# Kernel tuning notes

Measured on AMD Instinct MI355X. Metric: run time of the kernel, lower is better.

## Reference

```python
import jax, jax.numpy as jnp
import numpy as np

N = 100000   # nodes
E = 1600000  # edges
C = 128      # num_features == out_channels
L = 3        # num_layers


def setup_inputs() -> dict:
    key = jax.random.key(0)
    ks = jax.random.split(key, 7)
    x = jax.random.normal(ks[0], (N, C), dtype=jnp.float32)
    edge_index = jax.random.randint(ks[1], (2, E), 0, N, dtype=jnp.int64)
    # GatedGraphConv per-layer linear weights [L, C, C]
    weight = jax.random.normal(ks[2], (L, C, C), dtype=jnp.float32) / np.sqrt(C)
    # shared GRUCell params (torch layout: [3C, C] rows = r, z, n)
    w_ih = jax.random.normal(ks[3], (3 * C, C), dtype=jnp.float32) / np.sqrt(C)
    w_hh = jax.random.normal(ks[4], (3 * C, C), dtype=jnp.float32) / np.sqrt(C)
    b_ih = jax.random.normal(ks[5], (3 * C,), dtype=jnp.float32) * 0.01
    b_hh = jax.random.normal(ks[6], (3 * C,), dtype=jnp.float32) * 0.01
    return {"x": x, "edge_index": edge_index, "weight": weight,
            "w_ih": w_ih, "w_hh": w_hh, "b_ih": b_ih, "b_hh": b_hh}


def _gru_cell(inp, h, w_ih, w_hh, b_ih, b_hh):
    gi = inp @ w_ih.T + b_ih  # [N, 3C]
    gh = h @ w_hh.T + b_hh    # [N, 3C]
    i_r, i_z, i_n = jnp.split(gi, 3, axis=1)
    h_r, h_z, h_n = jnp.split(gh, 3, axis=1)
    r = jax.nn.sigmoid(i_r + h_r)
    z = jax.nn.sigmoid(i_z + h_z)
    n = jnp.tanh(i_n + r * h_n)
    return (1.0 - z) * n + z * h


def reference(x, edge_index, weight, w_ih, w_hh, b_ih, b_hh):
    src, dst = edge_index[0], edge_index[1]
    n_nodes = x.shape[0]
    # mean aggregation denominators (in-degree, 0-degree nodes -> 0 output)
    counts = jax.ops.segment_sum(jnp.ones(src.shape[0], dtype=x.dtype), dst,
                                 num_segments=n_nodes)
    denom = jnp.maximum(counts, 1.0)[:, None]
    h = x
    for i in range(weight.shape[0]):
        m = h @ weight[i]                                   # [N, C]
        agg = jax.ops.segment_sum(m[src], dst, num_segments=n_nodes) / denom
        h = _gru_cell(agg, h, w_ih, w_hh, b_ih, b_hh)
    # x.mean(1).unsqueeze(1) -> [N, 1], then tanh
    return jnp.tanh(jnp.mean(h, axis=1, keepdims=True))
```

## Files before the change

### kernel.cpp

```cpp
#include <hip/hip_runtime.h>
#include <math.h>

#define NN 100000
#define NE 1600000
#define CC 128
#define C3 384
#define SCAN_B 256
#define SCAN_NB ((NN + SCAN_B - 1) / SCAN_B)

typedef __attribute__((ext_vector_type(4))) float f4;
typedef __attribute__((ext_vector_type(8))) short s8;

__device__ __forceinline__ float sigmoidf_(float x) { return 1.0f / (1.0f + __expf(-x)); }
__device__ __forceinline__ float tanhf_(float x) { return 2.0f / (1.0f + __expf(-2.0f * x)) - 1.0f; }

__device__ __forceinline__ short f2bf(float x) {
    unsigned u = __float_as_uint(x);
    unsigned r = (u + 0x7fffu + ((u >> 16) & 1u)) >> 16;
    return (short)r;
}
__device__ __forceinline__ float bf2f(short s) {
    return __uint_as_float(((unsigned)(unsigned short)s) << 16);
}

__device__ __forceinline__ int detect_flag(const int* e32) {
    int allz = 1;
#pragma unroll
    for (int i = 0; i < 32; i++)
        if (e32[2 * i + 1] != 0) allz = 0;
    return allz;
}

__device__ __forceinline__ int edge_val(const void* edges, int f, long long idx) {
    return f ? (int)((const long long*)edges)[idx] : ((const int*)edges)[idx];
}

__global__ void k_count(const void* __restrict__ edges, int* __restrict__ counts) {
    __shared__ int sf;
    if (threadIdx.x == 0) sf = detect_flag((const int*)edges);
    __syncthreads();
    int f = sf;
    int e = blockIdx.x * blockDim.x + threadIdx.x;
    if (e < NE) {
        int d = edge_val(edges, f, (long long)NE + e);
        atomicAdd(&counts[d], 1);
    }
}

__global__ void k_scan1(const int* __restrict__ counts, int* __restrict__ bsum) {
    __shared__ int red[4];
    int t = threadIdx.x;
    int i = blockIdx.x * SCAN_B + t;
    int v = (i < NN) ? counts[i] : 0;
#pragma unroll
    for (int off = 32; off; off >>= 1) v += __shfl_down(v, off);
    if ((t & 63) == 0) red[t >> 6] = v;
    __syncthreads();
    if (t == 0) bsum[blockIdx.x] = red[0] + red[1] + red[2] + red[3];
}

__global__ void k_scan2(const int* __restrict__ bsum, int* __restrict__ boff,
                        int* __restrict__ coarse_cursor) {
    __shared__ int lds[512];
    int t = threadIdx.x;
    int v = (t < SCAN_NB) ? bsum[t] : 0;
    lds[t] = v;
    __syncthreads();
    for (int off = 1; off < 512; off <<= 1) {
        int u = (t >= off) ? lds[t - off] : 0;
        __syncthreads();
        lds[t] += u;
        __syncthreads();
    }
    if (t < SCAN_NB) {
        int ex = lds[t] - v;
        boff[t] = ex;
        coarse_cursor[t] = ex;
    }
}

__global__ void k_scan3(const int* __restrict__ counts, const int* __restrict__ boff,
                        int* __restrict__ rowptr, float* __restrict__ inv_denom) {
    __shared__ int lds[SCAN_B];
    int t = threadIdx.x;
    int i = blockIdx.x * SCAN_B + t;
    int v = (i < NN) ? counts[i] : 0;
    lds[t] = v;
    __syncthreads();
    for (int off = 1; off < SCAN_B; off <<= 1) {
        int u = (t >= off) ? lds[t - off] : 0;
        __syncthreads();
        lds[t] += u;
        __syncthreads();
    }
    if (i < NN) {
        rowptr[i] = boff[blockIdx.x] + lds[t] - v;
        inv_denom[i] = 1.0f / (float)((v > 1) ? v : 1);
    }
    if (i == 0) rowptr[NN] = NE;
}

__global__ __launch_bounds__(1024) void k_part(const void* __restrict__ edges,
                                               int* __restrict__ coarse_cursor,
                                               uint2* __restrict__ tmp) {
    __shared__ int hist[SCAN_NB];
    __shared__ int base[SCAN_NB];
    __shared__ int sf;
    int t = threadIdx.x;
    if (t == 0) sf = detect_flag((const int*)edges);
    long long e0 = (long long)blockIdx.x * 8192;

    for (int c = t; c < SCAN_NB; c += 1024) hist[c] = 0;
    __syncthreads();
    int f = sf;

    int src[8], dst[8];
#pragma unroll
    for (int i = 0; i < 8; i++) {
        long long e = e0 + i * 1024 + t;
        if (e < NE) {
            src[i] = edge_val(edges, f, e);
            dst[i] = edge_val(edges, f, NE + e);
            atomicAdd(&hist[dst[i] >> 8], 1);
        } else {
            dst[i] = -1;
        }
    }
    __syncthreads();
    for (int c = t; c < SCAN_NB; c += 1024) {
        int h = hist[c];
        base[c] = (h > 0) ? atomicAdd(&coarse_cursor[c], h) : 0;
        hist[c] = 0;
    }
    __syncthreads();
#pragma unroll
    for (int i = 0; i < 8; i++) {
        if (dst[i] >= 0) {
            int c = dst[i] >> 8;
            int off = atomicAdd(&hist[c], 1);
            tmp[base[c] + off] = make_uint2((unsigned)src[i], (unsigned)dst[i]);
        }
    }
}

__global__ void k_fine(const uint2* __restrict__ tmp, const int* __restrict__ rowptr,
                       int* __restrict__ csr_src) {
    __shared__ int cur[256];
    int c = blockIdx.x;
    int t = threadIdx.x;
    int d = c * 256 + t;
    cur[t] = (d <= NN) ? rowptr[d < NN ? d : NN] : NE;
    __syncthreads();
    int start = rowptr[c * 256];
    int endd = (c * 256 + 256 <= NN) ? rowptr[c * 256 + 256] : NE;
    for (int p = start + t; p < endd; p += 256) {
        uint2 pr = tmp[p];
        int slot = atomicAdd(&cur[pr.y & 255], 1);
        csr_src[slot] = (int)pr.x;
    }
}

__global__ void k_prep(const float* __restrict__ weight, const float* __restrict__ w_ih,
                       const float* __restrict__ w_hh, const float* __restrict__ b_ih,
                       const float* __restrict__ b_hh,
                       short* __restrict__ B1hi, short* __restrict__ B2hi,
                       float* __restrict__ bvec) {
    const int P1 = 3 * C3 * CC;
    int gid = blockIdx.x * blockDim.x + threadIdx.x;
    if (gid < P1) {
        int i = gid / (C3 * CC);
        int rem = gid % (C3 * CC);
        int j = rem / CC;
        int k = rem % CC;
        const float* Wr = weight + i * CC * CC + k * CC;
        const float* ir = w_ih + j * CC;
        float v = 0.f;
#pragma unroll 4
        for (int c = 0; c < CC; c++) v += Wr[c] * ir[c];
        short hi = f2bf(v);
        if (j < 256) B1hi[i * 65536 + j * 256 + k] = hi;
        else B2hi[i * 32768 + (j - 256) * 128 + k] = hi;
    } else if (gid < 2 * P1) {
        int g = gid - P1;
        int i = g / (C3 * CC);
        int rem = g % (C3 * CC);
        int j = rem / CC;
        int k = rem % CC;
        short hi = f2bf(w_hh[j * CC + k]);
        if (j < 256) B1hi[i * 65536 + j * 256 + 128 + k] = hi;
        else B2hi[i * 32768 + (j - 256 + 128) * 128 + k] = hi;
    } else if (gid < 2 * P1 + 512) {
        int j = gid - 2 * P1;
        float v;
        if (j < 256) v = b_ih[j] + b_hh[j];
        else if (j < 384) v = b_ih[j];
        else v = b_hh[j - 128];
        bvec[j] = v;
    }
}

__global__ void k_cvt(const float* __restrict__ x, unsigned short* __restrict__ hhi,
                      unsigned short* __restrict__ hlo) {
    long long g = ((long long)blockIdx.x * 256 + threadIdx.x) * 8;
    float4 v0 = *(const float4*)(x + g);
    float4 v1 = *(const float4*)(x + g + 4);
    float f[8] = {v0.x, v0.y, v0.z, v0.w, v1.x, v1.y, v1.z, v1.w};
    s8 oh, ol;
#pragma unroll
    for (int q = 0; q < 8; q++) {
        short hi = f2bf(f[q]);
        oh[q] = hi;
        ol[q] = f2bf(f[q] - bf2f(hi));
    }
    *(s8*)(hhi + g) = oh;
    *(s8*)(hlo + g) = ol;
}

__global__ __launch_bounds__(512, 8) void k_fused(
    const unsigned short* __restrict__ hhi_i, const unsigned short* __restrict__ hlo_i,
    unsigned short* __restrict__ hhi_o, unsigned short* __restrict__ hlo_o,
    const int* __restrict__ rowptr, const int* __restrict__ csr_src,
    const float* __restrict__ inv_denom,
    const short* __restrict__ B1hi, const short* __restrict__ B2hi,
    const float* __restrict__ bvec, float* __restrict__ out) {
    __shared__ short Ahi[8192];
    __shared__ short Alo[8192];
    __shared__ float osum[32];
    int t = threadIdx.x;
    long long nb = (long long)blockIdx.x * 32;
    int wv = t >> 6;
    int L = t & 63;

    if (out && t < 32) osum[t] = 0.f;

    {
        int rr = t >> 4;
        int c = t & 15;
        int c4 = 16 + c;
        long long row = nb + rr;
        int off = (c4 >> 2) * 1024 + (rr >> 4) * 512 + (rr & 15) * 32 + (c4 & 3) * 8;
        long long gsrc = row * CC + c * 8;
        *(s8*)&Ahi[off] = *(const s8*)(hhi_i + gsrc);
        *(s8*)&Alo[off] = *(const s8*)(hlo_i + gsrc);
    }

    {
        int q = L >> 4;
        int l16 = L & 15;
        int rr = wv * 4 + q;
        long long rowc = nb + rr;
        int lo = rowptr[rowc], hi = rowptr[rowc + 1];
        float acc0[8] = {0, 0, 0, 0, 0, 0, 0, 0};
        float acc1[8] = {0, 0, 0, 0, 0, 0, 0, 0};
        int e = lo;
        for (; e + 3 < hi; e += 4) {
            int s0 = csr_src[e];
            int s1 = csr_src[e + 1];
            int s2 = csr_src[e + 2];
            int s3 = csr_src[e + 3];
            s8 v0 = ((const s8*)(hhi_i + (long long)s0 * CC))[l16];
            s8 v1 = ((const s8*)(hhi_i + (long long)s1 * CC))[l16];
            s8 v2 = ((const s8*)(hhi_i + (long long)s2 * CC))[l16];
            s8 v3 = ((const s8*)(hhi_i + (long long)s3 * CC))[l16];
#pragma unroll
            for (int k = 0; k < 8; k++) {
                acc0[k] += bf2f(v0[k]) + bf2f(v2[k]);
                acc1[k] += bf2f(v1[k]) + bf2f(v3[k]);
            }
        }
        for (; e + 1 < hi; e += 2) {
            int s0 = csr_src[e];
            int s1 = csr_src[e + 1];
            s8 v0 = ((const s8*)(hhi_i + (long long)s0 * CC))[l16];
            s8 v1 = ((const s8*)(hhi_i + (long long)s1 * CC))[l16];
#pragma unroll
            for (int k = 0; k < 8; k++) {
                acc0[k] += bf2f(v0[k]);
                acc1[k] += bf2f(v1[k]);
            }
        }
        if (e < hi) {
            int s0 = csr_src[e];
            s8 v0 = ((const s8*)(hhi_i + (long long)s0 * CC))[l16];
#pragma unroll
            for (int k = 0; k < 8; k++) acc0[k] += bf2f(v0[k]);
        }
        float inv = inv_denom[rowc];
        s8 vh, vl;
#pragma unroll
        for (int k = 0; k < 8; k++) {
            float f = (acc0[k] + acc1[k]) * inv;
            short hi16 = f2bf(f);
            vh[k] = hi16;
            vl[k] = f2bf(f - bf2f(hi16));
        }
        int off = (l16 >> 2) * 1024 + (rr >> 4) * 512 + (rr & 15) * 32 + (l16 & 3) * 8;
        *(s8*)&Ahi[off] = vh;
        *(s8*)&Alo[off] = vl;
    }
    __syncthreads();

    int lm = L & 15;
    int lq = L >> 4;
    int j = wv * 16 + lm;

    f4 aR[2], aZ[2], aN[2], aH[2];
    {
        float bR = bvec[j], bZ = bvec[128 + j], bN = bvec[256 + j], bH = bvec[384 + j];
#pragma unroll
        for (int ch = 0; ch < 2; ch++) {
            aR[ch] = (f4){bR, bR, bR, bR};
            aZ[ch] = (f4){bZ, bZ, bZ, bZ};
            aN[ch] = (f4){bN, bN, bN, bN};
            aH[ch] = (f4){bH, bH, bH, bH};
        }
    }

#pragma unroll
    for (int ks = 0; ks < 8; ks++) {
        int o1 = ks * 32 + lq * 8;
        s8 bRh = *(const s8*)(B1hi + j * 256 + o1);
        s8 bZh = *(const s8*)(B1hi + (128 + j) * 256 + o1);
        int rowG = (ks < 4) ? j : (128 + j);
        int o2 = (ks & 3) * 32 + lq * 8;
        s8 bGh = *(const s8*)(B2hi + rowG * 128 + o2);
#pragma unroll
        for (int ch = 0; ch < 2; ch++) {
            int aoff = ks * 1024 + ch * 512 + lm * 32 + lq * 8;
            s8 ah = *(const s8*)&Ahi[aoff];
            s8 al = *(const s8*)&Alo[aoff];
            aR[ch] = __builtin_amdgcn_mfma_f32_16x16x32_bf16(ah, bRh, aR[ch], 0, 0, 0);
            aR[ch] = __builtin_amdgcn_mfma_f32_16x16x32_bf16(al, bRh, aR[ch], 0, 0, 0);
            aZ[ch] = __builtin_amdgcn_mfma_f32_16x16x32_bf16(ah, bZh, aZ[ch], 0, 0, 0);
            aZ[ch] = __builtin_amdgcn_mfma_f32_16x16x32_bf16(al, bZh, aZ[ch], 0, 0, 0);
            if (ks < 4) {
                aN[ch] = __builtin_amdgcn_mfma_f32_16x16x32_bf16(ah, bGh, aN[ch], 0, 0, 0);
                aN[ch] = __builtin_amdgcn_mfma_f32_16x16x32_bf16(al, bGh, aN[ch], 0, 0, 0);
            } else {
                aH[ch] = __builtin_amdgcn_mfma_f32_16x16x32_bf16(ah, bGh, aH[ch], 0, 0, 0);
                aH[ch] = __builtin_amdgcn_mfma_f32_16x16x32_bf16(al, bGh, aH[ch], 0, 0, 0);
            }
        }
    }

    {
        int c4 = 16 + (j >> 3);
        int obase = (c4 >> 2) * 1024 + (c4 & 3) * 8 + (j & 7);
#pragma unroll
        for (int ch = 0; ch < 2; ch++) {
#pragma unroll
            for (int r = 0; r < 4; r++) {
                int node = ch * 16 + lq * 4 + r;
                int off = obase + ch * 512 + (node & 15) * 32;
                float hp = bf2f(Ahi[off]) + bf2f(Alo[off]);
                float rg = sigmoidf_(aR[ch][r]);
                float zg = sigmoidf_(aZ[ch][r]);
                float nv = tanhf_(aN[ch][r] + rg * aH[ch][r]);
                float val = (1.f - zg) * nv + zg * hp;
                long long gnode = nb + node;
                if (out) {
                    atomicAdd(&osum[node], val);
                } else {
                    long long gd = gnode * CC + j;
                    short vh = f2bf(val);
                    hhi_o[gd] = (unsigned short)vh;
                    hlo_o[gd] = (unsigned short)f2bf(val - bf2f(vh));
                }
            }
        }
    }
    if (out) {
        __syncthreads();
        if (t < 32)
            out[nb + t] = tanhf_(osum[t] * (1.0f / 128.0f));
    }
}

extern "C" void kernel_launch(void* const* d_in, const int* in_sizes, int n_in,
                              void* d_out, int out_size, void* d_ws, size_t ws_size,
                              hipStream_t stream) {
    const float* x = (const float*)d_in[0];
    const void* edges = d_in[1];
    const float* weight = (const float*)d_in[2];
    const float* w_ih = (const float*)d_in[3];
    const float* w_hh = (const float*)d_in[4];
    const float* b_ih = (const float*)d_in[5];
    const float* b_hh = (const float*)d_in[6];
    float* out = (float*)d_out;

    char* ws = (char*)d_ws;
    size_t off = 0;
    auto alloc = [&](size_t bytes) -> char* {
        char* p = ws + off;
        off += (bytes + 255) & ~(size_t)255;
        return p;
    };
    int* counts = (int*)alloc((size_t)NN * 4);
    int* rowptr = (int*)alloc((size_t)(NN + 1) * 4);
    int* csr_src = (int*)alloc((size_t)NE * 4);
    float* inv_den = (float*)alloc((size_t)NN * 4);
    int* bsum = (int*)alloc((size_t)SCAN_NB * 4);
    int* boff = (int*)alloc((size_t)SCAN_NB * 4);
    int* coarse_cursor = (int*)alloc((size_t)SCAN_NB * 4);
    uint2* tmp = (uint2*)alloc((size_t)NE * 8);
    short* B1hi = (short*)alloc((size_t)3 * 65536 * 2);
    short* B2hi = (short*)alloc((size_t)3 * 32768 * 2);
    float* bvec = (float*)alloc(512 * 4);
    unsigned short* hhi0 = (unsigned short*)alloc((size_t)NN * CC * 2);
    unsigned short* hlo0 = (unsigned short*)alloc((size_t)NN * CC * 2);
    unsigned short* hhi1 = (unsigned short*)alloc((size_t)NN * CC * 2);
    unsigned short* hlo1 = (unsigned short*)alloc((size_t)NN * CC * 2);

    hipMemsetAsync(counts, 0, (size_t)NN * 4, stream);

    k_count<<<(NE + 255) / 256, 256, 0, stream>>>(edges, counts);
    k_scan1<<<SCAN_NB, SCAN_B, 0, stream>>>(counts, bsum);
    k_scan2<<<1, 512, 0, stream>>>(bsum, boff, coarse_cursor);
    k_scan3<<<SCAN_NB, SCAN_B, 0, stream>>>(counts, boff, rowptr, inv_den);
    k_part<<<(NE + 8191) / 8192, 1024, 0, stream>>>(edges, coarse_cursor, tmp);
    k_fine<<<SCAN_NB, 256, 0, stream>>>(tmp, rowptr, csr_src);
    int prep_threads = 2 * 3 * C3 * CC + 512;
    k_prep<<<(prep_threads + 255) / 256, 256, 0, stream>>>(weight, w_ih, w_hh, b_ih, b_hh,
                                                           B1hi, B2hi, bvec);
    k_cvt<<<(NN * CC) / 2048, 256, 0, stream>>>(x, hhi0, hlo0);

    const int blocks = (NN + 31) / 32;
    unsigned short* hi_in = hhi0;  unsigned short* lo_in = hlo0;
    unsigned short* hi_out = hhi1; unsigned short* lo_out = hlo1;
    for (int i = 0; i < 3; i++) {
        float* outp = (i == 2) ? out : nullptr;
        k_fused<<<blocks, 512, 0, stream>>>(hi_in, lo_in, hi_out, lo_out,
                                            rowptr, csr_src, inv_den,
                                            B1hi + (size_t)i * 65536,
                                            B2hi + (size_t)i * 32768,
                                            bvec, outp);
        unsigned short* th = hi_in; hi_in = hi_out; hi_out = th;
        unsigned short* tl = lo_in; lo_in = lo_out; lo_out = tl;
    }
}
```

Measured before the change: 674.7 us.

## Sort CSR neighbor lists and make fused layer kernel grid-stride persistent

Adds a per-node insertion sort of CSR source indices so neighbor gathers access memory in ascending order, aiming for better cache locality. Converts the fused aggregation+GRU kernel into a grid-stride loop over 32-node chunks with a fixed block count, reducing block launch overhead. The sort adds a preprocessing kernel with heavy shared memory use, and the fixed grid may leave load imbalance.

```diff
diff --git a/kernel.cpp b/kernel.cpp
--- a/kernel.cpp
+++ b/kernel.cpp
@@ -7,6 +7,8 @@
 #define C3 384
 #define SCAN_B 256
 #define SCAN_NB ((NN + SCAN_B - 1) / SCAN_B)
+#define NCHUNK ((NN + 31) / 32)
+#define GEN_BLOCKS 1024
 
 typedef __attribute__((ext_vector_type(4))) float f4;
 typedef __attribute__((ext_vector_type(8))) short s8;
@@ -158,6 +160,29 @@
         int slot = atomicAdd(&cur[pr.y & 255], 1);
         csr_src[slot] = (int)pr.x;
     }
+}
+
+#define DEG_CAP 64
+__global__ __launch_bounds__(128) void k_sort(const int* __restrict__ rowptr,
+                                              int* __restrict__ csr_src) {
+    __shared__ int buf[DEG_CAP * 128];
+    int t = threadIdx.x;
+    int gid = blockIdx.x * 128 + t;
+    if (gid >= NN) return;
+    int lo = rowptr[gid], hi = rowptr[gid + 1];
+    int deg = hi - lo;
+    if (deg > DEG_CAP) deg = DEG_CAP;
+    for (int k = 0; k < deg; k++) buf[k * 128 + t] = csr_src[lo + k];
+    for (int i = 1; i < deg; i++) {
+        int v = buf[i * 128 + t];
+        int p = i - 1;
+        while (p >= 0 && buf[p * 128 + t] > v) {
+            buf[(p + 1) * 128 + t] = buf[p * 128 + t];
+            p--;
+        }
+        buf[(p + 1) * 128 + t] = v;
+    }
+    for (int k = 0; k < deg; k++) csr_src[lo + k] = buf[k * 128 + t];
 }
 
 __global__ void k_prep(const float* __restrict__ weight, const float* __restrict__ w_ih,
@@ -227,152 +252,155 @@
     __shared__ short Alo[8192];
     __shared__ float osum[32];
     int t = threadIdx.x;
-    long long nb = (long long)blockIdx.x * 32;
     int wv = t >> 6;
     int L = t & 63;
 
-    if (out && t < 32) osum[t] = 0.f;
-
-    {
-        int rr = t >> 4;
-        int c = t & 15;
-        int c4 = 16 + c;
-        long long row = nb + rr;
-        int off = (c4 >> 2) * 1024 + (rr >> 4) * 512 + (rr & 15) * 32 + (c4 & 3) * 8;
-        long long gsrc = row * CC + c * 8;
-        *(s8*)&Ahi[off] = *(const s8*)(hhi_i + gsrc);
-        *(s8*)&Alo[off] = *(const s8*)(hlo_i + gsrc);
-    }
-
-    {
-        int q = L >> 4;
-        int l16 = L & 15;
-        int rr = wv * 4 + q;
-        long long rowc = nb + rr;
-        int lo = rowptr[rowc], hi = rowptr[rowc + 1];
-        float acc0[8] = {0, 0, 0, 0, 0, 0, 0, 0};
-        float acc1[8] = {0, 0, 0, 0, 0, 0, 0, 0};
-        int e = lo;
-        for (; e + 3 < hi; e += 4) {
-            int s0 = csr_src[e];
-            int s1 = csr_src[e + 1];
-            int s2 = csr_src[e + 2];
-            int s3 = csr_src[e + 3];
-            s8 v0 = ((const s8*)(hhi_i + (long long)s0 * CC))[l16];
-            s8 v1 = ((const s8*)(hhi_i + (long long)s1 * CC))[l16];
-            s8 v2 = ((const s8*)(hhi_i + (long long)s2 * CC))[l16];
-            s8 v3 = ((const s8*)(hhi_i + (long long)s3 * CC))[l16];
+    for (int chunk = blockIdx.x; chunk < NCHUNK; chunk += GEN_BLOCKS) {
+        long long nb = (long long)chunk * 32;
+        __syncthreads();
+        if (out && t < 32) osum[t] = 0.f;
+
+        {
+            int rr = t >> 4;
+            int c = t & 15;
+            int c4 = 16 + c;
+            long long row = nb + rr;
+            int off = (c4 >> 2) * 1024 + (rr >> 4) * 512 + (rr & 15) * 32 + (c4 & 3) * 8;
+            long long gsrc = row * CC + c * 8;
+            *(s8*)&Ahi[off] = *(const s8*)(hhi_i + gsrc);
+            *(s8*)&Alo[off] = *(const s8*)(hlo_i + gsrc);
+        }
+
+        {
+            int q = L >> 4;
+            int l16 = L & 15;
+            int rr = wv * 4 + q;
+            long long rowc = nb + rr;
+            int lo = rowptr[rowc], hi = rowptr[rowc + 1];
+            float acc0[8] = {0, 0, 0, 0, 0, 0, 0, 0};
+            float acc1[8] = {0, 0, 0, 0, 0, 0, 0, 0};
+            int e = lo;
+            for (; e + 3 < hi; e += 4) {
+                int s0 = csr_src[e];
+                int s1 = csr_src[e + 1];
+                int s2 = csr_src[e + 2];
+                int s3 = csr_src[e + 3];
+                s8 v0 = ((const s8*)(hhi_i + (long long)s0 * CC))[l16];
+                s8 v1 = ((const s8*)(hhi_i + (long long)s1 * CC))[l16];
+                s8 v2 = ((const s8*)(hhi_i + (long long)s2 * CC))[l16];
+                s8 v3 = ((const s8*)(hhi_i + (long long)s3 * CC))[l16];
+#pragma unroll
+                for (int k = 0; k < 8; k++) {
+                    acc0[k] += bf2f(v0[k]) + bf2f(v2[k]);
+                    acc1[k] += bf2f(v1[k]) + bf2f(v3[k]);
+                }
+            }
+            for (; e + 1 < hi; e += 2) {
+                int s0 = csr_src[e];
+                int s1 = csr_src[e + 1];
+                s8 v0 = ((const s8*)(hhi_i + (long long)s0 * CC))[l16];
+                s8 v1 = ((const s8*)(hhi_i + (long long)s1 * CC))[l16];
+#pragma unroll
+                for (int k = 0; k < 8; k++) {
+                    acc0[k] += bf2f(v0[k]);
+                    acc1[k] += bf2f(v1[k]);
+                }
+            }
+            if (e < hi) {
+                int s0 = csr_src[e];
+                s8 v0 = ((const s8*)(hhi_i + (long long)s0 * CC))[l16];
+#pragma unroll
+                for (int k = 0; k < 8; k++) acc0[k] += bf2f(v0[k]);
+            }
+            float inv = inv_denom[rowc];
+            s8 vh, vl;
 #pragma unroll
             for (int k = 0; k < 8; k++) {
-                acc0[k] += bf2f(v0[k]) + bf2f(v2[k]);
-                acc1[k] += bf2f(v1[k]) + bf2f(v3[k]);
-            }
-        }
-        for (; e + 1 < hi; e += 2) {
-            int s0 = csr_src[e];
-            int s1 = csr_src[e + 1];
-            s8 v0 = ((const s8*)(hhi_i + (long long)s0 * CC))[l16];
-            s8 v1 = ((const s8*)(hhi_i + (long long)s1 * CC))[l16];
-#pragma unroll
-            for (int k = 0; k < 8; k++) {
-                acc0[k] += bf2f(v0[k]);
-                acc1[k] += bf2f(v1[k]);
-            }
-        }
-        if (e < hi) {
-            int s0 = csr_src[e];
-            s8 v0 = ((const s8*)(hhi_i + (long long)s0 * CC))[l16];
-#pragma unroll
-            for (int k = 0; k < 8; k++) acc0[k] += bf2f(v0[k]);
-        }
-        float inv = inv_denom[rowc];
-        s8 vh, vl;
-#pragma unroll
-        for (int k = 0; k < 8; k++) {
-            float f = (acc0[k] + acc1[k]) * inv;
-            short hi16 = f2bf(f);
-            vh[k] = hi16;
-            vl[k] = f2bf(f - bf2f(hi16));
-        }
-        int off = (l16 >> 2) * 1024 + (rr >> 4) * 512 + (rr & 15) * 32 + (l16 & 3) * 8;
-        *(s8*)&Ahi[off] = vh;
-        *(s8*)&Alo[off] = vl;
-    }
-    __syncthreads();
-
-    int lm = L & 15;
-    int lq = L >> 4;
-    int j = wv * 16 + lm;
-
-    f4 aR[2], aZ[2], aN[2], aH[2];
-    {
-        float bR = bvec[j], bZ = bvec[128 + j], bN = bvec[256 + j], bH = bvec[384 + j];
-#pragma unroll
-        for (int ch = 0; ch < 2; ch++) {
-            aR[ch] = (f4){bR, bR, bR, bR};
-            aZ[ch] = (f4){bZ, bZ, bZ, bZ};
-            aN[ch] = (f4){bN, bN, bN, bN};
-            aH[ch] = (f4){bH, bH, bH, bH};
-        }
-    }
-
-#pragma unroll
-    for (int ks = 0; ks < 8; ks++) {
-        int o1 = ks * 32 + lq * 8;
-        s8 bRh = *(const s8*)(B1hi + j * 256 + o1);
-        s8 bZh = *(const s8*)(B1hi + (128 + j) * 256 + o1);
-        int rowG = (ks < 4) ? j : (128 + j);
-        int o2 = (ks & 3) * 32 + lq * 8;
-        s8 bGh = *(const s8*)(B2hi + rowG * 128 + o2);
-#pragma unroll
-        for (int ch = 0; ch < 2; ch++) {
-            int aoff = ks * 1024 + ch * 512 + lm * 32 + lq * 8;
-            s8 ah = *(const s8*)&Ahi[aoff];
-            s8 al = *(const s8*)&Alo[aoff];
-            aR[ch] = __builtin_amdgcn_mfma_f32_16x16x32_bf16(ah, bRh, aR[ch], 0, 0, 0);
-            aR[ch] = __builtin_amdgcn_mfma_f32_16x16x32_bf16(al, bRh, aR[ch], 0, 0, 0);
-            aZ[ch] = __builtin_amdgcn_mfma_f32_16x16x32_bf16(ah, bZh, aZ[ch], 0, 0, 0);
-            aZ[ch] = __builtin_amdgcn_mfma_f32_16x16x32_bf16(al, bZh, aZ[ch], 0, 0, 0);
-            if (ks < 4) {
-                aN[ch] = __builtin_amdgcn_mfma_f32_16x16x32_bf16(ah, bGh, aN[ch], 0, 0, 0);
-                aN[ch] = __builtin_amdgcn_mfma_f32_16x16x32_bf16(al, bGh, aN[ch], 0, 0, 0);
-            } else {
-                aH[ch] = __builtin_amdgcn_mfma_f32_16x16x32_bf16(ah, bGh, aH[ch], 0, 0, 0);
-                aH[ch] = __builtin_amdgcn_mfma_f32_16x16x32_bf16(al, bGh, aH[ch], 0, 0, 0);
-            }
-        }
-    }
-
-    {
-        int c4 = 16 + (j >> 3);
-        int obase = (c4 >> 2) * 1024 + (c4 & 3) * 8 + (j & 7);
-#pragma unroll
-        for (int ch = 0; ch < 2; ch++) {
-#pragma unroll
-            for (int r = 0; r < 4; r++) {
-                int node = ch * 16 + lq * 4 + r;
-                int off = obase + ch * 512 + (node & 15) * 32;
-                float hp = bf2f(Ahi[off]) + bf2f(Alo[off]);
-                float rg = sigmoidf_(aR[ch][r]);
-                float zg = sigmoidf_(aZ[ch][r]);
-                float nv = tanhf_(aN[ch][r] + rg * aH[ch][r]);
-                float val = (1.f - zg) * nv + zg * hp;
-                long long gnode = nb + node;
-                if (out) {
-                    atomicAdd(&osum[node], val);
+                float f = (acc0[k] + acc1[k]) * inv;
+                short hi16 = f2bf(f);
+                vh[k] = hi16;
+                vl[k] = f2bf(f - bf2f(hi16));
+            }
+            int off = (l16 >> 2) * 1024 + (rr >> 4) * 512 + (rr & 15) * 32 + (l16 & 3) * 8;
+            *(s8*)&Ahi[off] = vh;
+            *(s8*)&Alo[off] = vl;
+        }
+        __syncthreads();
+
+        int lm = L & 15;
+        int lq = L >> 4;
+        int j = wv * 16 + lm;
+
+        f4 aR[2], aZ[2], aN[2], aH[2];
+        {
+            float bR = bvec[j], bZ = bvec[128 + j], bN = bvec[256 + j], bH = bvec[384 + j];
+#pragma unroll
+            for (int ch = 0; ch < 2; ch++) {
+                aR[ch] = (f4){bR, bR, bR, bR};
+                aZ[ch] = (f4){bZ, bZ, bZ, bZ};
+                aN[ch] = (f4){bN, bN, bN, bN};
+                aH[ch] = (f4){bH, bH, bH, bH};
+            }
+        }
+
+#pragma unroll
+        for (int ks = 0; ks < 8; ks++) {
+            int o1 = ks * 32 + lq * 8;
+            s8 bRh = *(const s8*)(B1hi + j * 256 + o1);
+            s8 bZh = *(const s8*)(B1hi + (128 + j) * 256 + o1);
+            int rowG = (ks < 4) ? j : (128 + j);
+            int o2 = (ks & 3) * 32 + lq * 8;
+            s8 bGh = *(const s8*)(B2hi + rowG * 128 + o2);
+#pragma unroll
+            for (int ch = 0; ch < 2; ch++) {
+                int aoff = ks * 1024 + ch * 512 + lm * 32 + lq * 8;
+                s8 ah = *(const s8*)&Ahi[aoff];
+                s8 al = *(const s8*)&Alo[aoff];
+                aR[ch] = __builtin_amdgcn_mfma_f32_16x16x32_bf16(ah, bRh, aR[ch], 0, 0, 0);
+                aR[ch] = __builtin_amdgcn_mfma_f32_16x16x32_bf16(al, bRh, aR[ch], 0, 0, 0);
+                aZ[ch] = __builtin_amdgcn_mfma_f32_16x16x32_bf16(ah, bZh, aZ[ch], 0, 0, 0);
+                aZ[ch] = __builtin_amdgcn_mfma_f32_16x16x32_bf16(al, bZh, aZ[ch], 0, 0, 0);
+                if (ks < 4) {
+                    aN[ch] = __builtin_amdgcn_mfma_f32_16x16x32_bf16(ah, bGh, aN[ch], 0, 0, 0);
+                    aN[ch] = __builtin_amdgcn_mfma_f32_16x16x32_bf16(al, bGh, aN[ch], 0, 0, 0);
                 } else {
-                    long long gd = gnode * CC + j;
-                    short vh = f2bf(val);
-                    hhi_o[gd] = (unsigned short)vh;
-                    hlo_o[gd] = (unsigned short)f2bf(val - bf2f(vh));
+                    aH[ch] = __builtin_amdgcn_mfma_f32_16x16x32_bf16(ah, bGh, aH[ch], 0, 0, 0);
+                    aH[ch] = __builtin_amdgcn_mfma_f32_16x16x32_bf16(al, bGh, aH[ch], 0, 0, 0);
                 }
             }
         }
-    }
-    if (out) {
-        __syncthreads();
-        if (t < 32)
-            out[nb + t] = tanhf_(osum[t] * (1.0f / 128.0f));
+
+        {
+            int c4 = 16 + (j >> 3);
+            int obase = (c4 >> 2) * 1024 + (c4 & 3) * 8 + (j & 7);
+#pragma unroll
+            for (int ch = 0; ch < 2; ch++) {
+#pragma unroll
+                for (int r = 0; r < 4; r++) {
+                    int node = ch * 16 + lq * 4 + r;
+                    int off = obase + ch * 512 + (node & 15) * 32;
+                    float hp = bf2f(Ahi[off]) + bf2f(Alo[off]);
+                    float rg = sigmoidf_(aR[ch][r]);
+                    float zg = sigmoidf_(aZ[ch][r]);
+                    float nv = tanhf_(aN[ch][r] + rg * aH[ch][r]);
+                    float val = (1.f - zg) * nv + zg * hp;
+                    long long gnode = nb + node;
+                    if (out) {
+                        atomicAdd(&osum[(unsigned)node], val);
+                    } else {
+                        long long gd = gnode * CC + j;
+                        short vh = f2bf(val);
+                        hhi_o[gd] = (unsigned short)vh;
+                        hlo_o[gd] = (unsigned short)f2bf(val - bf2f(vh));
+                    }
+                }
+            }
+        }
+        if (out) {
+            __syncthreads();
+            if (t < 32)
+                out[nb + t] = tanhf_(osum[t] * (1.0f / 128.0f));
+        }
     }
 }
 
@@ -419,21 +447,21 @@
     k_scan3<<<SCAN_NB, SCAN_B, 0, stream>>>(counts, boff, rowptr, inv_den);
     k_part<<<(NE + 8191) / 8192, 1024, 0, stream>>>(edges, coarse_cursor, tmp);
     k_fine<<<SCAN_NB, 256, 0, stream>>>(tmp, rowptr, csr_src);
+    k_sort<<<(NN + 127) / 128, 128, 0, stream>>>(rowptr, csr_src);
     int prep_threads = 2 * 3 * C3 * CC + 512;
     k_prep<<<(prep_threads + 255) / 256, 256, 0, stream>>>(weight, w_ih, w_hh, b_ih, b_hh,
                                                            B1hi, B2hi, bvec);
     k_cvt<<<(NN * CC) / 2048, 256, 0, stream>>>(x, hhi0, hlo0);
 
-    const int blocks = (NN + 31) / 32;
     unsigned short* hi_in = hhi0;  unsigned short* lo_in = hlo0;
     unsigned short* hi_out = hhi1; unsigned short* lo_out = hlo1;
     for (int i = 0; i < 3; i++) {
         float* outp = (i == 2) ? out : nullptr;
-        k_fused<<<blocks, 512, 0, stream>>>(hi_in, lo_in, hi_out, lo_out,
-                                            rowptr, csr_src, inv_den,
-                                            B1hi + (size_t)i * 65536,
-                                            B2hi + (size_t)i * 32768,
-                                            bvec, outp);
+        k_fused<<<GEN_BLOCKS, 512, 0, stream>>>(hi_in, lo_in, hi_out, lo_out,
+                                                rowptr, csr_src, inv_den,
+                                                B1hi + (size_t)i * 65536,
+                                                B2hi + (size_t)i * 32768,
+                                                bvec, outp);
         unsigned short* th = hi_in; hi_in = hi_out; hi_out = th;
         unsigned short* tl = lo_in; lo_in = lo_out; lo_out = tl;
     }
```

Result: slower. 1.194 ms (+77.0%).
